# Kernel tuning notes

Hardware: AMD Instinct MI355X
Metric: run time of the kernel (lower is better)

Reference implementation:

```python
import jax, jax.numpy as jnp
import numpy as np

N, V, D_RAW, D_FEAT, G, NUM_CLASSES = 16, 12, 200704, 1024, 8, 40


def setup_inputs() -> dict:
    key = jax.random.key(0)
    ks = jax.random.split(key, 16)
    s = 0.02
    raw_feats = jax.random.normal(ks[0], (N, V, D_RAW), dtype=jnp.float32)
    final_views = jax.random.normal(ks[1], (N, V, D_FEAT), dtype=jnp.float32)
    rand_view_num = jax.random.randint(ks[2], (N,), 1, V + 1)
    # score FC: Linear(200704,256)+ReLU, Linear(256,1)+ReLU
    W1 = jax.random.normal(ks[3], (D_RAW, 256), dtype=jnp.float32) * s
    b1 = jnp.zeros((256,), jnp.float32)
    W2 = jax.random.normal(ks[4], (256, 1), dtype=jnp.float32) * s
    b2 = jnp.zeros((1,), jnp.float32)
    # classifier head
    Wf1 = jax.random.normal(ks[5], (D_FEAT, 512), dtype=jnp.float32) * s
    bf1 = jnp.zeros((512,), jnp.float32)
    Wf2 = jax.random.normal(ks[6], (512, 256), dtype=jnp.float32) * s
    bf2 = jnp.zeros((256,), jnp.float32)
    Wl = jax.random.normal(ks[7], (256, NUM_CLASSES), dtype=jnp.float32) * s
    bl = jnp.zeros((NUM_CLASSES,), jnp.float32)
    return {"raw_feats": raw_feats, "final_views": final_views,
            "rand_view_num": rand_view_num,
            "W1": W1, "b1": b1, "W2": W2, "b2": b2,
            "Wf1": Wf1, "bf1": bf1, "Wf2": Wf2, "bf2": bf2,
            "Wl": Wl, "bl": bl}


def _gvcnn_head(raw_feats, final_views, mask, W1, b1, W2, b2, Wf1, bf1, Wf2, bf2, Wl, bl):
    # view scores: FC(raw) -> sigmoid(tanh(abs(.)))
    h = jax.nn.relu(jnp.einsum('nvd,dk->nvk', raw_feats, W1) + b1)
    sraw = jax.nn.relu(h @ W2 + b2)[..., 0]                      # [N, V]
    score = jax.nn.sigmoid(jnp.tanh(jnp.abs(sraw)))              # in (0.5, 0.732)
    # bucket by score into G uniform bins on [0,1): bin = floor(score*G)
    bins = jnp.clip(jnp.floor(score * G).astype(jnp.int32), 0, G - 1)
    onehot = jax.nn.one_hot(bins, G, dtype=score.dtype) * mask[..., None]   # [N, V, G]
    counts = onehot.sum(axis=1)                                  # [N, G]
    safe_cnt = jnp.maximum(counts, 1.0)
    # per-bin mean view feature
    bin_sum = jnp.einsum('nvg,nvd->ngd', onehot, final_views)    # [N, G, D]
    bin_mean = bin_sum / safe_cnt[..., None]
    # per-bin weight: mean over bin members of ceil(score * n_bin)
    w = jnp.ceil(score[:, :, None] * counts[:, None, :]) * onehot  # [N, V, G]
    weight = (w.sum(axis=1) / safe_cnt) * (counts > 0)           # [N, G]
    # weighted fusion of non-empty bins
    desc = jnp.einsum('ng,ngd->nd', weight, bin_mean) / weight.sum(axis=1, keepdims=True)
    # classifier (dropout = identity in eval)
    out = jax.nn.relu(desc @ Wf1 + bf1)
    out = jax.nn.relu(out @ Wf2 + bf2)
    return out @ Wl + bl                                         # [N, num_classes]


def reference(raw_feats, final_views, rand_view_num, W1, b1, W2, b2, Wf1, bf1, Wf2, bf2, Wl, bl):
    mask = (jnp.arange(V)[None, :] < rand_view_num[:, None]).astype(raw_feats.dtype)  # [N, V]
    return _gvcnn_head(raw_feats, final_views, mask, W1, b1, W2, b2, Wf1, bf1, Wf2, bf2, Wl, bl)
```

## Files before the change

### kernel.cpp

```cpp
#include <hip/hip_runtime.h>
#include <math.h>

#define NB 16
#define NV 12
#define NROWS 192
#define DRAW 200704
#define KOUT 256
#define DFEAT 1024
#define NG 8
#define NCLS 40

#define NCHUNK 256
#define KC 784

#define ABASE 0
#define BBASE 24576

#define WS_SCORE 0
#define WS_PART  4096

typedef __attribute__((ext_vector_type(8))) short short8;
typedef __attribute__((ext_vector_type(16))) float f32x16;

__device__ __forceinline__ void cvt4(float4 v, uint2& hi, uint2& lo) {
    unsigned b0 = __float_as_uint(v.x), b1 = __float_as_uint(v.y);
    unsigned b2 = __float_as_uint(v.z), b3 = __float_as_uint(v.w);
    hi.x = (b0 >> 16) | (b1 & 0xffff0000u);
    hi.y = (b2 >> 16) | (b3 & 0xffff0000u);
    float r0 = v.x - __uint_as_float(b0 & 0xffff0000u);
    float r1 = v.y - __uint_as_float(b1 & 0xffff0000u);
    float r2 = v.z - __uint_as_float(b2 & 0xffff0000u);
    float r3 = v.w - __uint_as_float(b3 & 0xffff0000u);
    lo.x = (__float_as_uint(r0) >> 16) | (__float_as_uint(r1) & 0xffff0000u);
    lo.y = (__float_as_uint(r2) >> 16) | (__float_as_uint(r3) & 0xffff0000u);
}

#define K1_LOAD(DA, DB, S1)                                                    \
  {                                                                            \
    const int koff = (S1) * 32;                                                \
    _Pragma("unroll") for (int p = 0; p < 3; ++p) {                            \
      bool ok = aact[p] && (akq[p] * 4 + koff < KC);                           \
      DA[p] = ok ? *(const float4*)(aptr[p] + koff)                            \
                 : make_float4(0.f, 0.f, 0.f, 0.f);                            \
    }                                                                          \
    _Pragma("unroll") for (int q = 0; q < 16; ++q) {                           \
      int dd = ks + q + koff;                                                  \
      DB[q] = (dd < KC) ? bptr[(size_t)(koff + q) * KOUT] : 0.f;               \
    }                                                                          \
  }

#define K1_WRITE(CA, CB)                                                       \
  {                                                                            \
    _Pragma("unroll") for (int p = 0; p < 3; ++p) {                            \
      uint2 hi, lo; cvt4(CA[p], hi, lo);                                       \
      *(uint2*)(smem + awoff[p]) = hi;                                         \
      *(uint2*)(smem + awoff[p] + 1024) = lo;                                  \
    }                                                                          \
    _Pragma("unroll") for (int og = 0; og < 2; ++og) {                         \
      uint2 h0, l0, h1, l1;                                                    \
      cvt4(make_float4(CB[og*8+0], CB[og*8+1], CB[og*8+2], CB[og*8+3]), h0, l0); \
      cvt4(make_float4(CB[og*8+4], CB[og*8+5], CB[og*8+6], CB[og*8+7]), h1, l1); \
      uint4 hv; hv.x = h0.x; hv.y = h0.y; hv.z = h1.x; hv.w = h1.y;            \
      uint4 lv; lv.x = l0.x; lv.y = l0.y; lv.z = l1.x; lv.w = l1.y;            \
      *(uint4*)(smem + bwoff[og]) = hv;                                        \
      *(uint4*)(smem + bwoff[og] + 1024) = lv;                                 \
    }                                                                          \
  }

#define K1_MMA()                                                               \
  {                                                                            \
    _Pragma("unroll") for (int kf = 0; kf < 2; ++kf) {                         \
      short8 ah[3], al[3];                                                     \
      _Pragma("unroll") for (int tm = 0; tm < 3; ++tm) {                       \
        int off = ABASE + (wm * 3 + tm) * 4096 + kf * 2048 + (lane << 4);      \
        ah[tm] = *(const short8*)(smem + off);                                 \
        al[tm] = *(const short8*)(smem + off + 1024);                          \
      }                                                                        \
      _Pragma("unroll") for (int tn = 0; tn < 2; ++tn) {                       \
        int off = BBASE + (wn * 2 + tn) * 4096 + kf * 2048 + (lane << 4);      \
        short8 bh = *(const short8*)(smem + off);                              \
        short8 bl = *(const short8*)(smem + off + 1024);                       \
        _Pragma("unroll") for (int tm = 0; tm < 3; ++tm) {                     \
          acc[tm][tn] = __builtin_amdgcn_mfma_f32_32x32x16_bf16(ah[tm], bh, acc[tm][tn], 0, 0, 0); \
          acc[tm][tn] = __builtin_amdgcn_mfma_f32_32x32x16_bf16(ah[tm], bl, acc[tm][tn], 0, 0, 0); \
          acc[tm][tn] = __builtin_amdgcn_mfma_f32_32x32x16_bf16(al[tm], bh, acc[tm][tn], 0, 0, 0); \
        }                                                                      \
      }                                                                        \
    }                                                                          \
  }

#define K1_STEP(CA, CB, NA, NB_, S, DOLOAD)                                    \
  {                                                                            \
    __builtin_amdgcn_sched_barrier(0);                                         \
    __builtin_amdgcn_s_barrier();                                              \
    __builtin_amdgcn_sched_barrier(0);                                         \
    if (DOLOAD) K1_LOAD(NA, NB_, (S) + 1);                                     \
    K1_WRITE(CA, CB);                                                          \
    asm volatile("s_waitcnt lgkmcnt(0)" ::: "memory");                         \
    __builtin_amdgcn_s_barrier();                                              \
    __builtin_amdgcn_sched_barrier(0);                                         \
    K1_MMA();                                                                  \
  }

__global__ __launch_bounds__(512, 2)
void k1_mfma(const float* __restrict__ raw, const float* __restrict__ W1,
             const int* __restrict__ vnum, float* __restrict__ part)
{
    __shared__ __align__(16) char smem[57344];
    __shared__ char act[NROWS];
    const int t = threadIdx.x;
    const int c = blockIdx.x;
    const int d0 = c * KC;
    if (t < NROWS) act[t] = ((t % NV) < vnum[t / NV]) ? 1 : 0;
    __syncthreads();

    int akq[3];
    bool aact[3];
    const float* aptr[3];
    int awoff[3];
#pragma unroll
    for (int p = 0; p < 3; ++p) {
        int idx = p * 512 + t;
        int row = idx >> 3, kq = idx & 7;
        akq[p] = kq;
        aact[p] = act[row] != 0;
        aptr[p] = raw + (size_t)row * DRAW + d0 + kq * 4;
        awoff[p] = ABASE + (row >> 5) * 4096 + (kq >> 2) * 2048
                 + (((row & 31) + ((kq >> 1) & 1) * 32) << 4) + ((kq & 1) << 3);
    }
    const int col = t & 255;
    const int khalf = t >> 8;
    const int ks = khalf * 16;
    const float* bptr = W1 + (size_t)(d0 + ks) * KOUT + col;
    int bwoff[2];
#pragma unroll
    for (int og = 0; og < 2; ++og)
        bwoff[og] = BBASE + ((col >> 5) << 12) + (khalf << 11)
                  + (((col & 31) + og * 32) << 4);

    const int lane = t & 63;
    const int wave = t >> 6;
    const int wm = wave >> 2, wn = wave & 3;

    f32x16 acc[3][2];
#pragma unroll
    for (int i = 0; i < 3; ++i)
#pragma unroll
        for (int j = 0; j < 2; ++j)
#pragma unroll
            for (int r = 0; r < 16; ++r) acc[i][j][r] = 0.f;

    float4 A0[3], A1[3];
    float B0r[16], B1r[16];
    K1_LOAD(A0, B0r, 0);

#pragma unroll 1
    for (int sp = 0; sp < 12; ++sp) {
        K1_STEP(A0, B0r, A1, B1r, 2 * sp, 1);
        K1_STEP(A1, B1r, A0, B0r, 2 * sp + 1, 1);
    }
    K1_STEP(A0, B0r, A1, B1r, 24, 0);

    const int l31 = lane & 31, lh = lane >> 5;
#pragma unroll
    for (int tm = 0; tm < 3; ++tm) {
        int rowb = wm * 96 + tm * 32 + 4 * lh;
#pragma unroll
        for (int tn = 0; tn < 2; ++tn) {
            int colx = wn * 64 + tn * 32 + l31;
            f32x16 a = acc[tm][tn];
#pragma unroll
            for (int r = 0; r < 16; ++r) {
                int grow = rowb + (r & 3) + 8 * (r >> 2);
                part[((size_t)grow * NCHUNK + c) * KOUT + colx] = a[r];
            }
        }
    }
}

__global__ __launch_bounds__(1024)
void k2_score(const float* __restrict__ part, const float* __restrict__ b1,
              const float* __restrict__ W2, const float* __restrict__ b2,
              float* __restrict__ score)
{
    const int row = blockIdx.x, t = threadIdx.x;
    const int col = t & 255, cg = t >> 8;
    __shared__ float red[4][KOUT];
    __shared__ float r2[4];
    const float* p = part + ((size_t)row * NCHUNK + cg * 64) * KOUT + col;
    float s = 0.f;
#pragma unroll 8
    for (int i = 0; i < 64; ++i) s += p[(size_t)i * KOUT];
    red[cg][col] = s;
    __syncthreads();
    if (t < 256) {
        float v = red[0][col] + red[1][col] + red[2][col] + red[3][col];
        float h = fmaxf(v + b1[col], 0.f) * W2[col];
        for (int o = 32; o > 0; o >>= 1) h += __shfl_down(h, o, 64);
        if ((t & 63) == 0) r2[t >> 6] = h;
    }
    __syncthreads();
    if (t == 0) {
        float sm = r2[0] + r2[1] + r2[2] + r2[3];
        float sraw = fmaxf(sm + b2[0], 0.f);
        score[row] = 1.f / (1.f + expf(-tanhf(fabsf(sraw))));
    }
}

__global__ __launch_bounds__(512)
void k5f(const float* __restrict__ score, const int* __restrict__ vnum,
         const float* __restrict__ fv,
         const float* __restrict__ Wf1, const float* __restrict__ bf1,
         const float* __restrict__ Wf2, const float* __restrict__ bf2,
         const float* __restrict__ Wl,  const float* __restrict__ bl,
         float* __restrict__ out)
{
    const int n = blockIdx.x, t = threadIdx.x;
    __shared__ float coeffL[NV], descL[DFEAT], z1L[512], z2L[256];
    __shared__ float wsum[NG], wt[NG], outred[8][NCLS];
    __shared__ int cnt[NG];
    __shared__ float wtotS;
    if (t < NG) { cnt[t] = 0; wsum[t] = 0.f; }
    __syncthreads();
    const int vn = vnum[n];
    const bool act = (t < NV) && (t < vn);
    float sc = 0.f; int b = 0;
    if (act) {
        sc = score[n * NV + t];
        b = (int)floorf(sc * 8.f); b = b < 0 ? 0 : (b > 7 ? 7 : b);
        atomicAdd(&cnt[b], 1);
    }
    __syncthreads();
    if (act) atomicAdd(&wsum[b], ceilf(sc * (float)cnt[b]));
    __syncthreads();
    if (t < NG) wt[t] = (cnt[t] > 0) ? wsum[t] / (float)cnt[t] : 0.f;
    __syncthreads();
    if (t == 0) { float x = 0.f; for (int g = 0; g < NG; ++g) x += wt[g]; wtotS = x; }
    __syncthreads();
    if (t < NV) coeffL[t] = act ? wt[b] / ((float)cnt[b] * wtotS) : 0.f;
    __syncthreads();
#pragma unroll
    for (int p = 0; p < 2; ++p) {
        int d = t + p * 512;
        float a = 0.f;
#pragma unroll
        for (int v = 0; v < NV; ++v)
            a = fmaf(coeffL[v], fv[((size_t)n * NV + v) * DFEAT + d], a);
        descL[d] = a;
    }
    __syncthreads();
    {
        float a = 0.f;
#pragma unroll 8
        for (int d = 0; d < DFEAT; ++d)
            a = fmaf(descL[d], Wf1[(size_t)d * 512 + t], a);
        z1L[t] = fmaxf(a + bf1[t], 0.f);
    }
    __syncthreads();
    if (t < 256) {
        float a = 0.f;
#pragma unroll 8
        for (int d = 0; d < 512; ++d)
            a = fmaf(z1L[d], Wf2[(size_t)d * 256 + t], a);
        z2L[t] = fmaxf(a + bf2[t], 0.f);
    }
    __syncthreads();
    if (t < 320) {
        int j = t % NCLS, seg = t / NCLS;
        float a = 0.f;
#pragma unroll
        for (int dd = 0; dd < 32; ++dd) {
            int d = seg * 32 + dd;
            a = fmaf(z2L[d], Wl[d * NCLS + j], a);
        }
        outred[seg][j] = a;
    }
    __syncthreads();
    if (t < NCLS) {
        float a = bl[t];
#pragma unroll
        for (int s8 = 0; s8 < 8; ++s8) a += outred[s8][t];
        out[n * NCLS + t] = a;
    }
}

extern "C" void kernel_launch(void* const* d_in, const int* in_sizes, int n_in,
                              void* d_out, int out_size, void* d_ws, size_t ws_size,
                              hipStream_t stream)
{
    const float* raw  = (const float*)d_in[0];
    const float* fv   = (const float*)d_in[1];
    const int*   vnum = (const int*)d_in[2];
    const float* W1   = (const float*)d_in[3];
    const float* b1   = (const float*)d_in[4];
    const float* W2   = (const float*)d_in[5];
    const float* b2   = (const float*)d_in[6];
    const float* Wf1  = (const float*)d_in[7];
    const float* bf1  = (const float*)d_in[8];
    const float* Wf2  = (const float*)d_in[9];
    const float* bf2  = (const float*)d_in[10];
    const float* Wl   = (const float*)d_in[11];
    const float* bl   = (const float*)d_in[12];
    float* out = (float*)d_out;
    char* ws = (char*)d_ws;
    float* score = (float*)(ws + WS_SCORE);
    float* part  = (float*)(ws + WS_PART);

    k1_mfma<<<NCHUNK, 512, 0, stream>>>(raw, W1, vnum, part);
    k2_score<<<NROWS, 1024, 0, stream>>>(part, b1, W2, b2, score);
    k5f<<<NB, 512, 0, stream>>>(score, vnum, fv, Wf1, bf1, Wf2, bf2, Wl, bl, out);
}
```

Baseline: 180.3 us.

## Load W1 tiles as float4 rows and defer bf16 split to MMA stage

The W1 tile is now loaded with coalesced float4 loads along the output dimension instead of 16 scalar strided loads per thread, and stored raw as fp32 into shared memory. The hi/lo bf16 split of B is moved from the shared-memory write phase into the MMA loop, where each wave reads scalar fp32 values and converts them per fragment. This cuts global load instruction count and register pressure on the streaming W1 path. The cost is redundant conversion work, since the B conversion is repeated by the two wm waves, plus more LDS read instructions and possible bank conflicts in the inner MMA loop.

```diff
diff --git a/kernel.cpp b/kernel.cpp
--- a/kernel.cpp
+++ b/kernel.cpp
@@ -35,17 +35,24 @@
     lo.y = (__float_as_uint(r2) >> 16) | (__float_as_uint(r3) & 0xffff0000u);
 }
 
+__device__ __forceinline__ short8 mk8(uint2 a, uint2 b) {
+    union { unsigned u[4]; short8 s; } x;
+    x.u[0] = a.x; x.u[1] = a.y; x.u[2] = b.x; x.u[3] = b.y;
+    return x.s;
+}
+
 #define K1_LOAD(DA, DB, S1)                                                    \
   {                                                                            \
     const int koff = (S1) * 32;                                                \
+    const float4 f4z = make_float4(0.f, 0.f, 0.f, 0.f);                        \
     _Pragma("unroll") for (int p = 0; p < 3; ++p) {                            \
       bool ok = aact[p] && (akq[p] * 4 + koff < KC);                           \
-      DA[p] = ok ? *(const float4*)(aptr[p] + koff)                            \
-                 : make_float4(0.f, 0.f, 0.f, 0.f);                            \
+      DA[p] = ok ? *(const float4*)(aptr[p] + koff) : f4z;                     \
     }                                                                          \
-    _Pragma("unroll") for (int q = 0; q < 16; ++q) {                           \
-      int dd = ks + q + koff;                                                  \
-      DB[q] = (dd < KC) ? bptr[(size_t)(koff + q) * KOUT] : 0.f;               \
+    _Pragma("unroll") for (int p = 0; p < 4; ++p) {                            \
+      bool ok = (koff + p * 8 + bkk) < KC;                                     \
+      DB[p] = ok ? *(const float4*)(bptr + (size_t)(koff + p * 8) * KOUT)      \
+                 : f4z;                                                        \
     }                                                                          \
   }
 
@@ -56,15 +63,8 @@
       *(uint2*)(smem + awoff[p]) = hi;                                         \
       *(uint2*)(smem + awoff[p] + 1024) = lo;                                  \
     }                                                                          \
-    _Pragma("unroll") for (int og = 0; og < 2; ++og) {                         \
-      uint2 h0, l0, h1, l1;                                                    \
-      cvt4(make_float4(CB[og*8+0], CB[og*8+1], CB[og*8+2], CB[og*8+3]), h0, l0); \
-      cvt4(make_float4(CB[og*8+4], CB[og*8+5], CB[og*8+6], CB[og*8+7]), h1, l1); \
-      uint4 hv; hv.x = h0.x; hv.y = h0.y; hv.z = h1.x; hv.w = h1.y;            \
-      uint4 lv; lv.x = l0.x; lv.y = l0.y; lv.z = l1.x; lv.w = l1.y;            \
-      *(uint4*)(smem + bwoff[og]) = hv;                                        \
-      *(uint4*)(smem + bwoff[og] + 1024) = lv;                                 \
-    }                                                                          \
+    _Pragma("unroll") for (int p = 0; p < 4; ++p)                              \
+      *(float4*)(smem + bwoff + p * 8192) = CB[p];                             \
   }
 
 #define K1_MMA()                                                               \
@@ -77,9 +77,15 @@
         al[tm] = *(const short8*)(smem + off + 1024);                          \
       }                                                                        \
       _Pragma("unroll") for (int tn = 0; tn < 2; ++tn) {                       \
-        int off = BBASE + (wn * 2 + tn) * 4096 + kf * 2048 + (lane << 4);      \
-        short8 bh = *(const short8*)(smem + off);                              \
-        short8 bl = *(const short8*)(smem + off + 1024);                       \
+        float bq0[4], bq1[4];                                                  \
+        _Pragma("unroll") for (int q = 0; q < 4; ++q) {                        \
+          bq0[q] = *(const float*)(smem + bro + kf * 16384 + tn * 128 + q * 1024); \
+          bq1[q] = *(const float*)(smem + bro + kf * 16384 + tn * 128 + (q + 4) * 1024); \
+        }                                                                      \
+        uint2 h0, l0, h1, l1;                                                  \
+        cvt4(make_float4(bq0[0], bq0[1], bq0[2], bq0[3]), h0, l0);             \
+        cvt4(make_float4(bq1[0], bq1[1], bq1[2], bq1[3]), h1, l1);             \
+        short8 bh = mk8(h0, h1), bl = mk8(l0, l1);                             \
         _Pragma("unroll") for (int tm = 0; tm < 3; ++tm) {                     \
           acc[tm][tn] = __builtin_amdgcn_mfma_f32_32x32x16_bf16(ah[tm], bh, acc[tm][tn], 0, 0, 0); \
           acc[tm][tn] = __builtin_amdgcn_mfma_f32_32x32x16_bf16(ah[tm], bl, acc[tm][tn], 0, 0, 0); \
@@ -128,19 +134,14 @@
         awoff[p] = ABASE + (row >> 5) * 4096 + (kq >> 2) * 2048
                  + (((row & 31) + ((kq >> 1) & 1) * 32) << 4) + ((kq & 1) << 3);
     }
-    const int col = t & 255;
-    const int khalf = t >> 8;
-    const int ks = khalf * 16;
-    const float* bptr = W1 + (size_t)(d0 + ks) * KOUT + col;
-    int bwoff[2];
-#pragma unroll
-    for (int og = 0; og < 2; ++og)
-        bwoff[og] = BBASE + ((col >> 5) << 12) + (khalf << 11)
-                  + (((col & 31) + og * 32) << 4);
+    const int bkk = t >> 6;
+    const float* bptr = W1 + (size_t)(d0 + bkk) * KOUT + ((t & 63) << 2);
+    const int bwoff = BBASE + (bkk << 10) + ((t & 63) << 4);
 
     const int lane = t & 63;
     const int wave = t >> 6;
     const int wm = wave >> 2, wn = wave & 3;
+    const int bro = BBASE + ((lane >> 5) << 13) + ((wn * 64 + (lane & 31)) << 2);
 
     f32x16 acc[3][2];
 #pragma unroll
@@ -151,7 +152,7 @@
             for (int r = 0; r < 16; ++r) acc[i][j][r] = 0.f;
 
     float4 A0[3], A1[3];
-    float B0r[16], B1r[16];
+    float4 B0r[4], B1r[4];
     K1_LOAD(A0, B0r, 0);
 
 #pragma unroll 1
```

Result: slower. 244.4 us (+35.5%).

## Split score reduction and classifier head across more blocks

Applied to the files above, without the earlier changes.

The partial-sum reduction is split into two halves per row, doubling the block count. The score finalisation moves into a new kernel that runs four blocks per sample, each computing a 128-column slice of the first classifier layer with a 4-way K split. The remaining layers go to a separate small kernel. This spreads the weight reads of the head over more CUs, at the cost of an extra launch, redundant score and descriptor work in each of the four blocks, and an intermediate round-trip through global memory.

```diff
diff --git a/kernel.cpp b/kernel.cpp
--- a/kernel.cpp
+++ b/kernel.cpp
@@ -16,8 +16,9 @@
 #define ABASE 0
 #define BBASE 24576
 
-#define WS_SCORE 0
-#define WS_PART  4096
+#define WS_PART 0
+#define WS_HR   50331648
+#define WS_Z1   50724864
 
 typedef __attribute__((ext_vector_type(8))) short short8;
 typedef __attribute__((ext_vector_type(16))) float f32x16;
@@ -179,54 +180,60 @@
 }
 
 __global__ __launch_bounds__(1024)
-void k2_score(const float* __restrict__ part, const float* __restrict__ b1,
-              const float* __restrict__ W2, const float* __restrict__ b2,
-              float* __restrict__ score)
-{
-    const int row = blockIdx.x, t = threadIdx.x;
+void k2_half(const float* __restrict__ part, float* __restrict__ hr)
+{
+    const int row = blockIdx.x >> 1, half = blockIdx.x & 1, t = threadIdx.x;
     const int col = t & 255, cg = t >> 8;
     __shared__ float red[4][KOUT];
-    __shared__ float r2[4];
-    const float* p = part + ((size_t)row * NCHUNK + cg * 64) * KOUT + col;
+    const float* p = part + ((size_t)row * NCHUNK + half * 128 + cg * 32) * KOUT + col;
     float s = 0.f;
 #pragma unroll 8
-    for (int i = 0; i < 64; ++i) s += p[(size_t)i * KOUT];
+    for (int i = 0; i < 32; ++i) s += p[(size_t)i * KOUT];
     red[cg][col] = s;
     __syncthreads();
-    if (t < 256) {
-        float v = red[0][col] + red[1][col] + red[2][col] + red[3][col];
-        float h = fmaxf(v + b1[col], 0.f) * W2[col];
-        for (int o = 32; o > 0; o >>= 1) h += __shfl_down(h, o, 64);
-        if ((t & 63) == 0) r2[t >> 6] = h;
-    }
-    __syncthreads();
-    if (t == 0) {
-        float sm = r2[0] + r2[1] + r2[2] + r2[3];
-        float sraw = fmaxf(sm + b2[0], 0.f);
-        score[row] = 1.f / (1.f + expf(-tanhf(fabsf(sraw))));
-    }
+    if (t < 256)
+        hr[((size_t)row * 2 + half) * KOUT + col] =
+            red[0][col] + red[1][col] + red[2][col] + red[3][col];
 }
 
 __global__ __launch_bounds__(512)
-void k5f(const float* __restrict__ score, const int* __restrict__ vnum,
-         const float* __restrict__ fv,
-         const float* __restrict__ Wf1, const float* __restrict__ bf1,
-         const float* __restrict__ Wf2, const float* __restrict__ bf2,
-         const float* __restrict__ Wl,  const float* __restrict__ bl,
-         float* __restrict__ out)
-{
-    const int n = blockIdx.x, t = threadIdx.x;
-    __shared__ float coeffL[NV], descL[DFEAT], z1L[512], z2L[256];
-    __shared__ float wsum[NG], wt[NG], outred[8][NCLS];
+void kA(const float* __restrict__ hr, const float* __restrict__ b1,
+        const float* __restrict__ W2, const float* __restrict__ b2,
+        const int* __restrict__ vnum, const float* __restrict__ fv,
+        const float* __restrict__ Wf1, const float* __restrict__ bf1,
+        float* __restrict__ z1)
+{
+    const int n = blockIdx.x >> 2;
+    const int js = (blockIdx.x & 3) * 128;
+    const int t = threadIdx.x;
+    __shared__ float red4[4], sc_s[NV], coeffL[NV], wsum[NG], wt[NG], wtotS;
     __shared__ int cnt[NG];
-    __shared__ float wtotS;
+    __shared__ float descL[DFEAT];
+    __shared__ float zred[4][128];
+    for (int v = 0; v < NV; ++v) {
+        if (t < 256) {
+            int row = n * NV + v;
+            float s = hr[((size_t)row * 2 + 0) * KOUT + t]
+                    + hr[((size_t)row * 2 + 1) * KOUT + t];
+            float val = fmaxf(s + b1[t], 0.f) * W2[t];
+            for (int o = 32; o > 0; o >>= 1) val += __shfl_down(val, o, 64);
+            if ((t & 63) == 0) red4[t >> 6] = val;
+        }
+        __syncthreads();
+        if (t == 0) {
+            float sm = red4[0] + red4[1] + red4[2] + red4[3];
+            float sraw = fmaxf(sm + b2[0], 0.f);
+            sc_s[v] = 1.f / (1.f + expf(-tanhf(fabsf(sraw))));
+        }
+        __syncthreads();
+    }
     if (t < NG) { cnt[t] = 0; wsum[t] = 0.f; }
     __syncthreads();
     const int vn = vnum[n];
     const bool act = (t < NV) && (t < vn);
     float sc = 0.f; int b = 0;
     if (act) {
-        sc = score[n * NV + t];
+        sc = sc_s[t];
         b = (int)floorf(sc * 8.f); b = b < 0 ? 0 : (b > 7 ? 7 : b);
         atomicAdd(&cnt[b], 1);
     }
@@ -250,12 +257,30 @@
     }
     __syncthreads();
     {
+        const int j = t & 127, kq = t >> 7;
         float a = 0.f;
 #pragma unroll 8
-        for (int d = 0; d < DFEAT; ++d)
-            a = fmaf(descL[d], Wf1[(size_t)d * 512 + t], a);
-        z1L[t] = fmaxf(a + bf1[t], 0.f);
-    }
+        for (int dd = 0; dd < 256; ++dd) {
+            int d = kq * 256 + dd;
+            a = fmaf(descL[d], Wf1[(size_t)d * 512 + js + j], a);
+        }
+        zred[kq][j] = a;
+    }
+    __syncthreads();
+    if (t < 128) {
+        float s = zred[0][t] + zred[1][t] + zred[2][t] + zred[3][t];
+        z1[n * 512 + js + t] = fmaxf(s + bf1[js + t], 0.f);
+    }
+}
+
+__global__ __launch_bounds__(512)
+void kB(const float* __restrict__ z1, const float* __restrict__ Wf2,
+        const float* __restrict__ bf2, const float* __restrict__ Wl,
+        const float* __restrict__ bl, float* __restrict__ out)
+{
+    const int n = blockIdx.x, t = threadIdx.x;
+    __shared__ float z1L[512], z2L[256], outred[8][NCLS];
+    z1L[t] = z1[n * 512 + t];
     __syncthreads();
     if (t < 256) {
         float a = 0.f;
@@ -303,10 +328,12 @@
     const float* bl   = (const float*)d_in[12];
     float* out = (float*)d_out;
     char* ws = (char*)d_ws;
-    float* score = (float*)(ws + WS_SCORE);
-    float* part  = (float*)(ws + WS_PART);
+    float* part = (float*)(ws + WS_PART);
+    float* hr   = (float*)(ws + WS_HR);
+    float* z1   = (float*)(ws + WS_Z1);
 
     k1_mfma<<<NCHUNK, 512, 0, stream>>>(raw, W1, vnum, part);
-    k2_score<<<NROWS, 1024, 0, stream>>>(part, b1, W2, b2, score);
-    k5f<<<NB, 512, 0, stream>>>(score, vnum, fv, Wf1, bf1, Wf2, bf2, Wl, bl, out);
-}
+    k2_half<<<2 * NROWS, 1024, 0, stream>>>(part, hr);
+    kA<<<4 * NB, 512, 0, stream>>>(hr, b1, W2, b2, vnum, fv, Wf1, bf1, z1);
+    kB<<<NB, 512, 0, stream>>>(z1, Wf2, bf2, Wl, bl, out);
+}
```

Result: faster. 148.5 us, median of 2 (-17.7%).
